# Kernel optimization log

Hardware: AMD Instinct MI355X
Metric: run time of the kernel (lower is better)

Reference implementation:

```python
import jax, jax.numpy as jnp
import numpy as np

B, C, C2, E = 4, 1024, 1024, 1024
D = 1024          # context_size (d_q = d_kv)
NH = 16           # module's n_heads arg -> actual head_dim after the quirky view
G = D // NH       # effective number of head groups = 64


def setup_inputs() -> dict:
    key = jax.random.key(0)
    ks = jax.random.split(key, 6)
    s = 0.02
    return {
        "x1": jax.random.normal(ks[0], (B, C, E), dtype=jnp.float32),
        "x2": jax.random.normal(ks[1], (B, C2, E), dtype=jnp.float32),
        "W_q": jax.random.normal(ks[2], (E, D), dtype=jnp.float32) * s,
        "W_k": jax.random.normal(ks[3], (E, D), dtype=jnp.float32) * s,
        "W_v": jax.random.normal(ks[4], (E, D), dtype=jnp.float32) * s,
        "W_o": jax.random.normal(ks[5], (D, D), dtype=jnp.float32) * s,
    }


def _split_heads(t):
    # (B, S, D) -> view (B, S, G, NH) -> transpose(1,2) -> (B, G, S, NH)
    b, s, _ = t.shape
    return jnp.transpose(t.reshape(b, s, G, NH), (0, 2, 1, 3))


def reference(x1, x2, W_q, W_k, W_v, W_o):
    Q = _split_heads(x1 @ W_q)   # (B, G, C, NH)
    K = _split_heads(x2 @ W_k)   # (B, G, C2, NH)
    V = _split_heads(x2 @ W_v)   # (B, G, C2, NH)
    scale = 1.0 / jnp.sqrt(jnp.asarray(NH, dtype=Q.dtype))
    scores = jnp.einsum("bgqh,bgkh->bgqk", Q, K) * scale  # (B, G, C, C2)
    w = jax.nn.softmax(scores, axis=-1)
    out = jnp.einsum("bgqk,bgkh->bgqh", w, V)             # (B, G, C, NH)
    out = jnp.transpose(out, (0, 2, 1, 3)).reshape(B, C, D)
    return out @ W_o  # dropout p=0 -> identity
```

## Files before the change

kernel.cpp:

```cpp
#include <hip/hip_runtime.h>


typedef _Float16 f16x8 __attribute__((ext_vector_type(8)));
typedef _Float16 f16x4 __attribute__((ext_vector_type(4)));
typedef _Float16 f16x2 __attribute__((ext_vector_type(2)));
typedef float    f32x4 __attribute__((ext_vector_type(4)));
typedef float    f32x16 __attribute__((ext_vector_type(16)));

#define GLOAD_LDS16(gp, lp)                                              \
    __builtin_amdgcn_global_load_lds(                                    \
        (const __attribute__((address_space(1))) void*)(gp),             \
        (__attribute__((address_space(3))) void*)(lp), 16, 0, 0)

static __device__ __forceinline__ f16x8 pack8f(const float* p) {
    f16x2 a = __builtin_bit_cast(f16x2, __builtin_amdgcn_cvt_pkrtz(p[0], p[1]));
    f16x2 b = __builtin_bit_cast(f16x2, __builtin_amdgcn_cvt_pkrtz(p[2], p[3]));
    f16x2 c = __builtin_bit_cast(f16x2, __builtin_amdgcn_cvt_pkrtz(p[4], p[5]));
    f16x2 d = __builtin_bit_cast(f16x2, __builtin_amdgcn_cvt_pkrtz(p[6], p[7]));
    f16x8 r;
    r[0] = a[0]; r[1] = a[1]; r[2] = b[0]; r[3] = b[1];
    r[4] = c[0]; r[5] = c[1]; r[6] = d[0]; r[7] = d[1];
    return r;
}

__global__ __launch_bounds__(256) void prep_kernel(
        const float* __restrict__ x1, const float* __restrict__ x2,
        const float* __restrict__ W0, const float* __restrict__ W1,
        const float* __restrict__ W2, const float* __restrict__ W3,
        _Float16* __restrict__ y1, _Float16* __restrict__ y2,
        _Float16* __restrict__ T0, _Float16* __restrict__ T1,
        _Float16* __restrict__ T2, _Float16* __restrict__ T3) {
    int bx = blockIdx.x, tid = threadIdx.x;
    if (bx < 8192) {
        int i = bx * 256 + tid;
        const float* x = (i < 1048576) ? x1 : x2;
        _Float16* y = (i < 1048576) ? y1 : y2;
        int j = i & 1048575;
        float4 v = ((const float4*)x)[j];
        f16x4 h = { (_Float16)v.x, (_Float16)v.y, (_Float16)v.z, (_Float16)v.w };
        ((f16x4*)y)[j] = h;
    } else {
        int z = (bx - 8192) >> 10;
        const float* W = (z == 0) ? W0 : (z == 1) ? W1 : (z == 2) ? W2 : W3;
        _Float16* WT = (z == 0) ? T0 : (z == 1) ? T1 : (z == 2) ? T2 : T3;
        int t = (bx - 8192) & 1023;
        int c0 = (t & 31) * 32, r0 = (t >> 5) * 32;
        __shared__ float tile[32][33];
        int tx = tid & 31, ty = tid >> 5;
#pragma unroll
        for (int i = 0; i < 32; i += 8)
            tile[ty + i][tx] = W[(r0 + ty + i) * 1024 + (c0 + tx)];
        __syncthreads();
#pragma unroll
        for (int i = 0; i < 32; i += 8)
            WT[(c0 + ty + i) * 1024 + (r0 + tx)] = (_Float16)tile[tx][ty + i];
    }
}

template <bool OUTF32>
static __device__ __forceinline__ void gemm_body(const _Float16* __restrict__ A,
                                                 const _Float16* __restrict__ BT,
                                                 void* __restrict__ Cout,
                                                 _Float16* As, _Float16* Bs) {
    const int tid = threadIdx.x, lane = tid & 63, wave = tid >> 6;
    const int wm = wave >> 1, wn = wave & 1;
    const int col = lane & 15, quad = lane >> 4;
    const int m0 = blockIdx.y * 128, n0 = blockIdx.x * 128;

    f32x4 acc[4][4];
#pragma unroll
    for (int i = 0; i < 4; i++)
#pragma unroll
        for (int j = 0; j < 4; j++) acc[i][j] = (f32x4){0.f, 0.f, 0.f, 0.f};

    const int srow = wave * 8 + (lane >> 3);
    const int sch = (lane & 7) * 8;
    const _Float16* Ag = A + (size_t)(m0 + srow) * 1024 + sch;
    const _Float16* Bg = BT + (size_t)(n0 + srow) * 1024 + sch;
    _Float16* Asl = As + wave * 512;
    _Float16* Bsl = Bs + wave * 512;

    for (int kt = 0; kt < 16; kt++) {
        __syncthreads();
#pragma unroll
        for (int c = 0; c < 4; c++) {
            GLOAD_LDS16(Ag + (size_t)(c * 32) * 1024 + kt * 64, Asl + c * 2048);
            GLOAD_LDS16(Bg + (size_t)(c * 32) * 1024 + kt * 64, Bsl + c * 2048);
        }
        __syncthreads();
#pragma unroll
        for (int ki = 0; ki < 2; ki++) {
            f16x8 af[4], bf[4];
#pragma unroll
            for (int i = 0; i < 4; i++)
                af[i] = *(const f16x8*)(As + (wm * 64 + i * 16 + col) * 64 + ki * 32 + quad * 8);
#pragma unroll
            for (int j = 0; j < 4; j++)
                bf[j] = *(const f16x8*)(Bs + (wn * 64 + j * 16 + col) * 64 + ki * 32 + quad * 8);
#pragma unroll
            for (int i = 0; i < 4; i++)
#pragma unroll
                for (int j = 0; j < 4; j++)
                    acc[i][j] = __builtin_amdgcn_mfma_f32_16x16x32_f16(af[i], bf[j], acc[i][j], 0, 0, 0);
        }
    }

#pragma unroll
    for (int i = 0; i < 4; i++)
#pragma unroll
        for (int ii = 0; ii < 4; ii++) {
            int row = m0 + wm * 64 + i * 16 + quad * 4 + ii;
#pragma unroll
            for (int j = 0; j < 4; j++) {
                int cc = n0 + wn * 64 + j * 16 + col;
                if (OUTF32) ((float*)Cout)[(size_t)row * 1024 + cc] = acc[i][j][ii];
                else ((_Float16*)Cout)[(size_t)row * 1024 + cc] = (_Float16)acc[i][j][ii];
            }
        }
}

__global__ __launch_bounds__(256, 3) void gemm_qkv_kernel(
        const _Float16* __restrict__ x1h, const _Float16* __restrict__ x2h,
        const _Float16* __restrict__ WqT, const _Float16* __restrict__ WkT,
        const _Float16* __restrict__ WvT,
        _Float16* __restrict__ Qh, _Float16* __restrict__ Kh, _Float16* __restrict__ Vh) {
    __shared__ _Float16 As[128 * 64], Bs[128 * 64];
    int z = blockIdx.z;
    const _Float16* A = (z == 0) ? x1h : x2h;
    const _Float16* BT = (z == 0) ? WqT : (z == 1) ? WkT : WvT;
    _Float16* C = (z == 0) ? Qh : (z == 1) ? Kh : Vh;
    gemm_body<false>(A, BT, (void*)C, As, Bs);
}

__global__ __launch_bounds__(256, 3) void gemm_wo_kernel(const _Float16* __restrict__ Ah,
                                                         const _Float16* __restrict__ WoT,
                                                         float* __restrict__ out) {
    __shared__ _Float16 As[128 * 64], Bs[128 * 64];
    gemm_body<true>(Ah, WoT, (void*)out, As, Bs);
}

__global__ __launch_bounds__(512, 8) void attn_kernel(const _Float16* __restrict__ Qh,
                                                      const _Float16* __restrict__ Kh,
                                                      const _Float16* __restrict__ Vh,
                                                      _Float16* __restrict__ Ah) {
    int pair = blockIdx.y;
    int b = pair >> 6, g = pair & 63;
    __shared__ _Float16 KA[8192];
    __shared__ _Float16 VA[8192];
    __shared__ _Float16 ones[8];

    const _Float16* Kg = Kh + (size_t)(b * 1024) * 1024 + g * 16;
    const _Float16* Vg = Vh + (size_t)(b * 1024) * 1024 + g * 16;
    int tid = threadIdx.x;
    if (tid < 8) ones[tid] = (_Float16)1.f;

    int lane = tid & 63, wave = tid >> 6;
    int n = lane & 31, h5 = lane >> 5;
    int q0 = blockIdx.x * 256 + wave * 32;

    f16x8 qf;
    {
        f16x8 t = *(const f16x8*)(Qh + (size_t)(b * 1024 + q0 + n) * 1024 + g * 16 + h5 * 8);
#pragma unroll
        for (int j = 0; j < 8; j++) qf[j] = (_Float16)((float)t[j] * 0.360673760f);
    }

    f32x16 acc = {0.f, 0.f, 0.f, 0.f, 0.f, 0.f, 0.f, 0.f,
                  0.f, 0.f, 0.f, 0.f, 0.f, 0.f, 0.f, 0.f};
    const f32x16 zero16 = acc;
    const _Float16* vbase = (n < 16) ? (VA + (n + 16 * h5) * 8) : ones;
    const int vstep = (n < 16) ? 256 : 0;

    for (int c = 0; c < 2; c++) {
        if (c) __syncthreads();
#pragma unroll
        for (int it = 0; it < 2; it++) {
            int row = it * 256 + (tid >> 1);
            int part = tid & 1;
            int pm = (row & 19) | ((row & 4) << 1) | ((row & 8) >> 1);
            *(uint4*)(KA + (((row >> 5) * 64) + pm + 32 * part) * 8) =
                *(const uint4*)(Kg + (size_t)(c * 512 + row) * 1024 + part * 8);
        }
#pragma unroll
        for (int it = 0; it < 2; it++) {
            int row = it * 256 + (tid >> 1);
            int part = tid & 1;
            f16x8 v = *(const f16x8*)(Vg + (size_t)(c * 512 + row) * 1024 + part * 8);
            int base = (row >> 4) * 256 + ((row >> 3) & 1) * 128 + part * 64 + (row & 7);
#pragma unroll
            for (int j = 0; j < 8; j++) VA[base + j * 8] = v[j];
        }
        __syncthreads();

#pragma unroll 2
        for (int t = 0; t < 16; t++) {
            f16x8 ak = *(const f16x8*)(KA + (t * 64 + lane) * 8);
            f32x16 s = __builtin_amdgcn_mfma_f32_32x32x16_f16(ak, qf, zero16, 0, 0, 0);
            float p[16];
#pragma unroll
            for (int i = 0; i < 16; i++) p[i] = __builtin_amdgcn_exp2f(s[i]);
            f16x8 pb0 = pack8f(p);
            f16x8 pb1 = pack8f(p + 8);
            f16x8 av0 = *(const f16x8*)(vbase + (2 * t) * vstep);
            f16x8 av1 = *(const f16x8*)(vbase + (2 * t + 1) * vstep);
            acc = __builtin_amdgcn_mfma_f32_32x32x16_f16(av0, pb0, acc, 0, 0, 0);
            acc = __builtin_amdgcn_mfma_f32_32x32x16_f16(av1, pb1, acc, 0, 0, 0);
        }
    }

    float rl = 1.0f / acc[8];
    f16x4 o0, o1;
#pragma unroll
    for (int i = 0; i < 4; i++) o0[i] = (_Float16)(acc[i] * rl);
#pragma unroll
    for (int i = 0; i < 4; i++) o1[i] = (_Float16)(acc[4 + i] * rl);
    _Float16* ob = Ah + (size_t)(b * 1024 + q0 + n) * 1024 + g * 16 + h5 * 4;
    *(f16x4*)(ob) = o0;
    *(f16x4*)(ob + 8) = o1;
}

extern "C" void kernel_launch(void* const* d_in, const int* in_sizes, int n_in,
                              void* d_out, int out_size, void* d_ws, size_t ws_size,
                              hipStream_t stream) {
    const float* x1 = (const float*)d_in[0];
    const float* x2 = (const float*)d_in[1];
    const float* Wq = (const float*)d_in[2];
    const float* Wk = (const float*)d_in[3];
    const float* Wv = (const float*)d_in[4];
    const float* Wo = (const float*)d_in[5];

    char* ws = (char*)d_ws;
    const size_t MB = 1u << 20;
    if (ws_size < 56 * MB) return;

    _Float16* x1h = (_Float16*)(ws + 0 * MB);
    _Float16* x2h = (_Float16*)(ws + 8 * MB);
    _Float16* WqT = (_Float16*)(ws + 16 * MB);
    _Float16* WkT = (_Float16*)(ws + 18 * MB);
    _Float16* WvT = (_Float16*)(ws + 20 * MB);
    _Float16* WoT = (_Float16*)(ws + 22 * MB);
    _Float16* Qh  = (_Float16*)(ws + 24 * MB);
    _Float16* Kh  = (_Float16*)(ws + 32 * MB);
    _Float16* Vh  = (_Float16*)(ws + 40 * MB);
    _Float16* Ah  = (_Float16*)(ws + 48 * MB);

    prep_kernel<<<12288, 256, 0, stream>>>(x1, x2, Wq, Wk, Wv, Wo,
                                           x1h, x2h, WqT, WkT, WvT, WoT);

    gemm_qkv_kernel<<<dim3(8, 32, 3), 256, 0, stream>>>(x1h, x2h, WqT, WkT, WvT, Qh, Kh, Vh);

    attn_kernel<<<dim3(4, 256), 512, 0, stream>>>(Qh, Kh, Vh, Ah);

    gemm_wo_kernel<<<dim3(8, 32), 256, 0, stream>>>(Ah, WoT, (float*)d_out);
}
```

Before: 197.9 us.

## Process two query tiles per wave in attention to reuse K/V LDS loads

Each attention wave now handles 64 queries (two 32-query groups) instead of 32, so the grid halves and each block stages K/V into LDS once for 512 queries instead of 256. The K and V fragments read from LDS are reused across both query groups. This halves global K/V traffic and LDS staging work per query, at the cost of more registers (two accumulators), a lower occupancy bound, and fewer blocks to fill the GPU.

```diff
diff --git a/kernel.cpp b/kernel.cpp
--- a/kernel.cpp
+++ b/kernel.cpp
@@ -139,7 +139,7 @@
     gemm_body<true>(Ah, WoT, (void*)out, As, Bs);
 }
 
-__global__ __launch_bounds__(512, 8) void attn_kernel(const _Float16* __restrict__ Qh,
+__global__ __launch_bounds__(512, 4) void attn_kernel(const _Float16* __restrict__ Qh,
                                                       const _Float16* __restrict__ Kh,
                                                       const _Float16* __restrict__ Vh,
                                                       _Float16* __restrict__ Ah) {
@@ -156,18 +156,23 @@
 
     int lane = tid & 63, wave = tid >> 6;
     int n = lane & 31, h5 = lane >> 5;
-    int q0 = blockIdx.x * 256 + wave * 32;
-
-    f16x8 qf;
-    {
-        f16x8 t = *(const f16x8*)(Qh + (size_t)(b * 1024 + q0 + n) * 1024 + g * 16 + h5 * 8);
-#pragma unroll
-        for (int j = 0; j < 8; j++) qf[j] = (_Float16)((float)t[j] * 0.360673760f);
-    }
-
-    f32x16 acc = {0.f, 0.f, 0.f, 0.f, 0.f, 0.f, 0.f, 0.f,
-                  0.f, 0.f, 0.f, 0.f, 0.f, 0.f, 0.f, 0.f};
-    const f32x16 zero16 = acc;
+    int q0 = blockIdx.x * 512 + wave * 64;
+
+    f16x8 qf[2];
+#pragma unroll
+    for (int qg = 0; qg < 2; qg++) {
+        f16x8 t = *(const f16x8*)(Qh + (size_t)(b * 1024 + q0 + qg * 32 + n) * 1024 +
+                                  g * 16 + h5 * 8);
+#pragma unroll
+        for (int j = 0; j < 8; j++) qf[qg][j] = (_Float16)((float)t[j] * 0.360673760f);
+    }
+
+    f32x16 acc[2];
+#pragma unroll
+    for (int qg = 0; qg < 2; qg++)
+        acc[qg] = (f32x16){0.f, 0.f, 0.f, 0.f, 0.f, 0.f, 0.f, 0.f,
+                           0.f, 0.f, 0.f, 0.f, 0.f, 0.f, 0.f, 0.f};
+    const f32x16 zero16 = acc[0];
     const _Float16* vbase = (n < 16) ? (VA + (n + 16 * h5) * 8) : ones;
     const int vstep = (n < 16) ? 256 : 0;
 
@@ -195,28 +200,34 @@
 #pragma unroll 2
         for (int t = 0; t < 16; t++) {
             f16x8 ak = *(const f16x8*)(KA + (t * 64 + lane) * 8);
-            f32x16 s = __builtin_amdgcn_mfma_f32_32x32x16_f16(ak, qf, zero16, 0, 0, 0);
-            float p[16];
-#pragma unroll
-            for (int i = 0; i < 16; i++) p[i] = __builtin_amdgcn_exp2f(s[i]);
-            f16x8 pb0 = pack8f(p);
-            f16x8 pb1 = pack8f(p + 8);
             f16x8 av0 = *(const f16x8*)(vbase + (2 * t) * vstep);
             f16x8 av1 = *(const f16x8*)(vbase + (2 * t + 1) * vstep);
-            acc = __builtin_amdgcn_mfma_f32_32x32x16_f16(av0, pb0, acc, 0, 0, 0);
-            acc = __builtin_amdgcn_mfma_f32_32x32x16_f16(av1, pb1, acc, 0, 0, 0);
-        }
-    }
-
-    float rl = 1.0f / acc[8];
-    f16x4 o0, o1;
-#pragma unroll
-    for (int i = 0; i < 4; i++) o0[i] = (_Float16)(acc[i] * rl);
-#pragma unroll
-    for (int i = 0; i < 4; i++) o1[i] = (_Float16)(acc[4 + i] * rl);
-    _Float16* ob = Ah + (size_t)(b * 1024 + q0 + n) * 1024 + g * 16 + h5 * 4;
-    *(f16x4*)(ob) = o0;
-    *(f16x4*)(ob + 8) = o1;
+#pragma unroll
+            for (int qg = 0; qg < 2; qg++) {
+                f32x16 s = __builtin_amdgcn_mfma_f32_32x32x16_f16(ak, qf[qg], zero16, 0, 0, 0);
+                float p[16];
+#pragma unroll
+                for (int i = 0; i < 16; i++) p[i] = __builtin_amdgcn_exp2f(s[i]);
+                f16x8 pb0 = pack8f(p);
+                f16x8 pb1 = pack8f(p + 8);
+                acc[qg] = __builtin_amdgcn_mfma_f32_32x32x16_f16(av0, pb0, acc[qg], 0, 0, 0);
+                acc[qg] = __builtin_amdgcn_mfma_f32_32x32x16_f16(av1, pb1, acc[qg], 0, 0, 0);
+            }
+        }
+    }
+
+#pragma unroll
+    for (int qg = 0; qg < 2; qg++) {
+        float rl = 1.0f / acc[qg][8];
+        f16x4 o0, o1;
+#pragma unroll
+        for (int i = 0; i < 4; i++) o0[i] = (_Float16)(acc[qg][i] * rl);
+#pragma unroll
+        for (int i = 0; i < 4; i++) o1[i] = (_Float16)(acc[qg][4 + i] * rl);
+        _Float16* ob = Ah + (size_t)(b * 1024 + q0 + qg * 32 + n) * 1024 + g * 16 + h5 * 4;
+        *(f16x4*)(ob) = o0;
+        *(f16x4*)(ob + 8) = o1;
+    }
 }
 
 extern "C" void kernel_launch(void* const* d_in, const int* in_sizes, int n_in,
@@ -249,7 +260,7 @@
 
     gemm_qkv_kernel<<<dim3(8, 32, 3), 256, 0, stream>>>(x1h, x2h, WqT, WkT, WvT, Qh, Kh, Vh);
 
-    attn_kernel<<<dim3(4, 256), 512, 0, stream>>>(Qh, Kh, Vh, Ah);
+    attn_kernel<<<dim3(2, 256), 512, 0, stream>>>(Qh, Kh, Vh, Ah);
 
     gemm_wo_kernel<<<dim3(8, 32), 256, 0, stream>>>(Ah, WoT, (float*)d_out);
 }
```

New measurement: 198.0 us. Within noise of the previous version (+0.1%).
